# Kernel tuning notes

Measured on AMD Instinct MI355X. Metric: run time of the kernel, lower is better.

## Reference

```python
import jax, jax.numpy as jnp
import numpy as np

GAMMA = 1.0


def setup_inputs() -> dict:
    key = jax.random.key(0)
    k1, k2, k3 = jax.random.split(key, 3)
    n_query, n_train, d = 8192, 8192, 512
    X = jax.random.normal(k1, (n_query, d), dtype=jnp.float32)
    train_X = jax.random.normal(k2, (n_train, d), dtype=jnp.float32)
    dual_coef = jax.random.normal(k3, (n_train,), dtype=jnp.float32)
    return {"X": X, "train_X": train_X, "dual_coef": dual_coef}


def _rbf_kernel(x, y, gamma):
    x2 = jnp.sum(x * x, axis=-1, keepdims=True)          # (n_x, 1)
    y2 = jnp.sum(y * y, axis=-1)[None, :]                # (1, n_y)
    sq_dist = x2 + y2 - 2.0 * jnp.einsum('qd,td->qt', x, y)
    sq_dist = jnp.maximum(sq_dist, 0.0)                  # guard tiny negatives
    return jnp.exp(-gamma * sq_dist)                     # (n_x, n_y)


def reference(X, train_X, dual_coef):
    K_test = _rbf_kernel(X, train_X, GAMMA)              # (n_query, n_train)
    return K_test @ dual_coef                            # (n_query,)
```

## Files before the change

### kernel.cpp

```cpp
#include <hip/hip_runtime.h>
#include <hip/hip_bf16.h>
#include <stdint.h>

#define NQ 8192
#define NT 8192
#define DIM 512
#define BK 32
#define NKT (DIM / BK)
#define BM 256
#define BN 256
#define BUF_ELEMS ((BM + BN) * BK)

typedef __hip_bfloat16 bf16;
using bf16x8  = __attribute__((ext_vector_type(8))) short;
using f32x4   = __attribute__((ext_vector_type(4))) float;
using short8v = __attribute__((ext_vector_type(8))) short;

typedef __attribute__((address_space(1))) void* gas1_t;
typedef __attribute__((address_space(3))) void* las3_t;

__global__ void zero_out_k(float* __restrict__ out) {
    out[blockIdx.x * 256 + threadIdx.x] = 0.0f;
}

__global__ void prep_k(const float* __restrict__ X, const float* __restrict__ T,
                       bf16* __restrict__ Xb, bf16* __restrict__ Tb,
                       float* __restrict__ x2, float* __restrict__ y2) {
    const int w    = threadIdx.x >> 6;
    const int lane = threadIdx.x & 63;
    const int wid  = blockIdx.x * 4 + w;
#pragma unroll
    for (int rr = 0; rr < 2; ++rr) {
        const int row = wid * 2 + rr;
        const float* src; bf16* dst; float* nrm; int r;
        if (row < NQ) { r = row;      src = X + (size_t)r * DIM; dst = Xb + (size_t)r * DIM; nrm = x2; }
        else          { r = row - NQ; src = T + (size_t)r * DIM; dst = Tb + (size_t)r * DIM; nrm = y2; }
        const float4 v0 = reinterpret_cast<const float4*>(src)[lane * 2];
        const float4 v1 = reinterpret_cast<const float4*>(src)[lane * 2 + 1];
        float s = v0.x*v0.x + v0.y*v0.y + v0.z*v0.z + v0.w*v0.w
                + v1.x*v1.x + v1.y*v1.y + v1.z*v1.z + v1.w*v1.w;
        short8v pk;
        pk[0] = (short)__bfloat16_as_ushort(__float2bfloat16(v0.x));
        pk[1] = (short)__bfloat16_as_ushort(__float2bfloat16(v0.y));
        pk[2] = (short)__bfloat16_as_ushort(__float2bfloat16(v0.z));
        pk[3] = (short)__bfloat16_as_ushort(__float2bfloat16(v0.w));
        pk[4] = (short)__bfloat16_as_ushort(__float2bfloat16(v1.x));
        pk[5] = (short)__bfloat16_as_ushort(__float2bfloat16(v1.y));
        pk[6] = (short)__bfloat16_as_ushort(__float2bfloat16(v1.z));
        pk[7] = (short)__bfloat16_as_ushort(__float2bfloat16(v1.w));
        reinterpret_cast<short8v*>(dst)[lane] = pk;
#pragma unroll
        for (int off = 32; off; off >>= 1) s += __shfl_xor(s, off, 64);
        if (lane == 0) nrm[r] = s;
    }
}

__device__ __forceinline__ void stage_tile(
    const bf16* __restrict__ Tb, const bf16* __restrict__ Xb,
    int tBlk, int qBlk, int kt, bf16* sA, bf16* sB, int w, int lane) {
    const int k0 = kt * BK;
    const int rl = lane >> 2;
    const int sw = (rl >> 1) & 3;
    const int c  = (lane & 3) ^ sw;
#pragma unroll
    for (int j = 0; j < 2; ++j) {
        const int R0 = j * 128 + w * 16;
        const int R  = R0 + rl;
        const bf16* ga = Tb + (size_t)(tBlk + R) * DIM + k0 + c * 8;
        __builtin_amdgcn_global_load_lds((gas1_t)ga, (las3_t)(sA + R0 * BK), 16, 0, 0);
        const bf16* gb = Xb + (size_t)(qBlk + R) * DIM + k0 + c * 8;
        __builtin_amdgcn_global_load_lds((gas1_t)gb, (las3_t)(sB + R0 * BK), 16, 0, 0);
    }
}

__device__ __forceinline__ void compute_tile(
    const bf16* sA, const bf16* sB, int wm, int wn, int lane, f32x4 (&acc)[8][4]) {
    const int fr = lane & 15;
    const int fc = lane >> 4;
    const int swz = (fc ^ ((fr >> 1) & 3)) * 8;
    bf16x8 a[8], b[4];
#pragma unroll
    for (int m = 0; m < 8; ++m) {
        const int R = wm * 128 + m * 16 + fr;
        a[m] = *reinterpret_cast<const bf16x8*>(sA + R * BK + swz);
    }
#pragma unroll
    for (int n = 0; n < 4; ++n) {
        const int R = wn * 64 + n * 16 + fr;
        b[n] = *reinterpret_cast<const bf16x8*>(sB + R * BK + swz);
    }
    __builtin_amdgcn_s_setprio(1);
#pragma unroll
    for (int m = 0; m < 8; ++m)
#pragma unroll
        for (int n = 0; n < 4; ++n)
            acc[m][n] = __builtin_amdgcn_mfma_f32_16x16x32_bf16(a[m], b[n], acc[m][n], 0, 0, 0);
    __builtin_amdgcn_s_setprio(0);
}

#define WAIT_BAR(N)                                              \
    asm volatile("s_waitcnt vmcnt(" #N ")" ::: "memory");        \
    __builtin_amdgcn_s_barrier();                                \
    __builtin_amdgcn_sched_barrier(0);

__global__ __launch_bounds__(512, 2) void krr_mfma_k(
    const bf16* __restrict__ Tb, const bf16* __restrict__ Xb,
    const float* __restrict__ x2, const float* __restrict__ y2,
    const float* __restrict__ coef, float* __restrict__ out) {

    __shared__ bf16 lds[3 * BUF_ELEMS];

    const int tid  = threadIdx.x;
    const int w    = tid >> 6;
    const int lane = tid & 63;
    const int wm   = w >> 2;
    const int wn   = w & 3;

    const int qBlk = blockIdx.x * BN;
    const int tBlk = blockIdx.y * BM;

    f32x4 acc[8][4];
    const f32x4 z4 = {0.f, 0.f, 0.f, 0.f};
#pragma unroll
    for (int m = 0; m < 8; ++m)
#pragma unroll
        for (int n = 0; n < 4; ++n) acc[m][n] = z4;

    stage_tile(Tb, Xb, tBlk, qBlk, 0, lds,             lds + BM * BK,             w, lane);
    stage_tile(Tb, Xb, tBlk, qBlk, 1, lds + BUF_ELEMS, lds + BUF_ELEMS + BM * BK, w, lane);

    int bc = 0, bs = 2;
    for (int t = 0; t < NKT - 2; ++t) {
        WAIT_BAR(4)
        stage_tile(Tb, Xb, tBlk, qBlk, t + 2,
                   lds + bs * BUF_ELEMS, lds + bs * BUF_ELEMS + BM * BK, w, lane);
        compute_tile(lds + bc * BUF_ELEMS, lds + bc * BUF_ELEMS + BM * BK, wm, wn, lane, acc);
        bc = (bc == 2) ? 0 : bc + 1;
        bs = (bs == 2) ? 0 : bs + 1;
    }
    WAIT_BAR(4)
    compute_tile(lds + bc * BUF_ELEMS, lds + bc * BUF_ELEMS + BM * BK, wm, wn, lane, acc);
    bc = (bc == 2) ? 0 : bc + 1;
    WAIT_BAR(0)
    compute_tile(lds + bc * BUF_ELEMS, lds + bc * BUF_ELEMS + BM * BK, wm, wn, lane, acc);

    float s[4], x2q[4];
#pragma unroll
    for (int n = 0; n < 4; ++n) {
        s[n]   = 0.f;
        x2q[n] = x2[qBlk + wn * 64 + n * 16 + (lane & 15)];
    }
#pragma unroll
    for (int m = 0; m < 8; ++m) {
        const int tb = tBlk + wm * 128 + m * 16 + ((lane >> 4) << 2);
        float y2v[4], cfv[4];
#pragma unroll
        for (int r = 0; r < 4; ++r) { y2v[r] = y2[tb + r]; cfv[r] = coef[tb + r]; }
#pragma unroll
        for (int n = 0; n < 4; ++n)
#pragma unroll
            for (int r = 0; r < 4; ++r) {
                const float d  = acc[m][n][r];
                const float sq = fmaxf(x2q[n] + y2v[r] - 2.0f * d, 0.f);
                s[n] += __expf(-sq) * cfv[r];
            }
    }
#pragma unroll
    for (int n = 0; n < 4; ++n) {
        float v = s[n];
        v += __shfl_xor(v, 16, 64);
        v += __shfl_xor(v, 32, 64);
        if (lane < 16) atomicAdd(&out[qBlk + wn * 64 + n * 16 + lane], v);
    }
}

__global__ void krr_naive_k(const float* __restrict__ X, const float* __restrict__ T,
                            const float* __restrict__ coef, float* __restrict__ out) {
    __shared__ float xq[DIM];
    const int q = blockIdx.x;
    for (int i = threadIdx.x; i < DIM; i += 256) xq[i] = X[(size_t)q * DIM + i];
    __syncthreads();
    float s2 = 0.f;
    for (int i = 0; i < DIM; ++i) s2 += xq[i] * xq[i];
    float acc = 0.f;
    for (int t = threadIdx.x; t < NT; t += 256) {
        const float* ty = T + (size_t)t * DIM;
        float dot = 0.f, yy = 0.f;
        for (int i = 0; i < DIM; ++i) { float yv = ty[i]; dot += xq[i] * yv; yy += yv * yv; }
        float sq = fmaxf(s2 + yy - 2.0f * dot, 0.f);
        acc += __expf(-sq) * coef[t];
    }
#pragma unroll
    for (int off = 32; off > 0; off >>= 1) acc += __shfl_down(acc, off, 64);
    __shared__ float red[4];
    if ((threadIdx.x & 63) == 0) red[threadIdx.x >> 6] = acc;
    __syncthreads();
    if (threadIdx.x == 0) out[q] = red[0] + red[1] + red[2] + red[3];
}

extern "C" void kernel_launch(void* const* d_in, const int* in_sizes, int n_in,
                              void* d_out, int out_size, void* d_ws, size_t ws_size,
                              hipStream_t stream) {
    const float* X    = (const float*)d_in[0];
    const float* T    = (const float*)d_in[1];
    const float* coef = (const float*)d_in[2];
    float* out = (float*)d_out;

    zero_out_k<<<NQ / 256, 256, 0, stream>>>(out);

    const size_t need = (size_t)(NQ + NT) * DIM * sizeof(bf16) + (size_t)(NQ + NT) * sizeof(float);
    if (ws_size >= need) {
        bf16* Xb  = (bf16*)d_ws;
        bf16* Tb  = Xb + (size_t)NQ * DIM;
        float* x2 = (float*)(Tb + (size_t)NT * DIM);
        float* y2 = x2 + NQ;
        prep_k<<<2048, 256, 0, stream>>>(X, T, Xb, Tb, x2, y2);
        dim3 grid(NQ / BN, NT / BM);
        krr_mfma_k<<<grid, 512, 0, stream>>>(Tb, Xb, x2, y2, coef, out);
    } else {
        krr_naive_k<<<NQ, 256, 0, stream>>>(X, T, coef, out);
    }
}
```

Baseline: 149.9 us.

## Switch to 32x32 MFMA with BK=64 double buffer and quadrant-interleaved staging

```diff
diff --git a/kernel.cpp b/kernel.cpp
--- a/kernel.cpp
+++ b/kernel.cpp
@@ -5,15 +5,14 @@
 #define NQ 8192
 #define NT 8192
 #define DIM 512
-#define BK 32
+#define BK 64
 #define NKT (DIM / BK)
 #define BM 256
 #define BN 256
-#define BUF_ELEMS ((BM + BN) * BK)
 
 typedef __hip_bfloat16 bf16;
 using bf16x8  = __attribute__((ext_vector_type(8))) short;
-using f32x4   = __attribute__((ext_vector_type(4))) float;
+using f32x16  = __attribute__((ext_vector_type(16))) float;
 using short8v = __attribute__((ext_vector_type(8))) short;
 
 typedef __attribute__((address_space(1))) void* gas1_t;
@@ -55,60 +54,122 @@
     }
 }
 
-__device__ __forceinline__ void stage_tile(
+__device__ __forceinline__ void stage_half(
+    const bf16* __restrict__ src, int rowBase, int kt, bf16* dstHalf, int w, int lane) {
+    const int k0 = kt * BK;
+    const int rl = lane >> 3;
+    const int cl = (lane & 7) ^ rl;
+#pragma unroll
+    for (int j = 0; j < 2; ++j) {
+        const int R0 = w * 16 + j * 8;
+        const bf16* g = src + (size_t)(rowBase + R0 + rl) * DIM + k0 + cl * 8;
+        __builtin_amdgcn_global_load_lds((gas1_t)g, (las3_t)(dstHalf + R0 * BK), 16, 0, 0);
+    }
+}
+
+__device__ __forceinline__ bf16x8 lds_frag(const bf16* buf, int row, int ks, int kg) {
+    const int cl = ks * 2 + kg;
+    return *reinterpret_cast<const bf16x8*>(buf + row * BK + ((cl ^ (row & 7)) << 3));
+}
+
+#define MFMA32(A, B, C) __builtin_amdgcn_mfma_f32_32x32x16_bf16(A, B, C, 0, 0, 0)
+
+template<bool ST12, bool ST34, int VMC>
+__device__ __forceinline__ void segment(
     const bf16* __restrict__ Tb, const bf16* __restrict__ Xb,
-    int tBlk, int qBlk, int kt, bf16* sA, bf16* sB, int w, int lane) {
-    const int k0 = kt * BK;
-    const int rl = lane >> 2;
-    const int sw = (rl >> 1) & 3;
-    const int c  = (lane & 3) ^ sw;
-#pragma unroll
-    for (int j = 0; j < 2; ++j) {
-        const int R0 = j * 128 + w * 16;
-        const int R  = R0 + rl;
-        const bf16* ga = Tb + (size_t)(tBlk + R) * DIM + k0 + c * 8;
-        __builtin_amdgcn_global_load_lds((gas1_t)ga, (las3_t)(sA + R0 * BK), 16, 0, 0);
-        const bf16* gb = Xb + (size_t)(qBlk + R) * DIM + k0 + c * 8;
-        __builtin_amdgcn_global_load_lds((gas1_t)gb, (las3_t)(sB + R0 * BK), 16, 0, 0);
-    }
-}
-
-__device__ __forceinline__ void compute_tile(
-    const bf16* sA, const bf16* sB, int wm, int wn, int lane, f32x4 (&acc)[8][4]) {
-    const int fr = lane & 15;
-    const int fc = lane >> 4;
-    const int swz = (fc ^ ((fr >> 1) & 3)) * 8;
-    bf16x8 a[8], b[4];
-#pragma unroll
-    for (int m = 0; m < 8; ++m) {
-        const int R = wm * 128 + m * 16 + fr;
-        a[m] = *reinterpret_cast<const bf16x8*>(sA + R * BK + swz);
-    }
-#pragma unroll
-    for (int n = 0; n < 4; ++n) {
-        const int R = wn * 64 + n * 16 + fr;
-        b[n] = *reinterpret_cast<const bf16x8*>(sB + R * BK + swz);
-    }
-    __builtin_amdgcn_s_setprio(1);
-#pragma unroll
-    for (int m = 0; m < 8; ++m)
-#pragma unroll
-        for (int n = 0; n < 4; ++n)
-            acc[m][n] = __builtin_amdgcn_mfma_f32_16x16x32_bf16(a[m], b[n], acc[m][n], 0, 0, 0);
-    __builtin_amdgcn_s_setprio(0);
-}
-
-#define WAIT_BAR(N)                                              \
-    asm volatile("s_waitcnt vmcnt(" #N ")" ::: "memory");        \
-    __builtin_amdgcn_s_barrier();                                \
-    __builtin_amdgcn_sched_barrier(0);
+    int tBlk, int qBlk, bf16* bufC, bf16* bufN, int s,
+    int wm, int wn, int w, int lane, f32x16 (&acc)[4][2]) {
+
+    const bf16* cA = bufC;
+    const bf16* cB = bufC + 16384;
+    bf16* nA = bufN;
+    bf16* nB = bufN + 16384;
+    const int l31 = lane & 31;
+    const int kg  = lane >> 5;
+
+    bf16x8 aF[2][4], b0[4], b1[4];
+
+#pragma unroll
+    for (int mi = 0; mi < 2; ++mi) {
+        const int row = wm * 64 + mi * 32 + l31;
+#pragma unroll
+        for (int ks = 0; ks < 4; ++ks) aF[mi][ks] = lds_frag(cA, row, ks, kg);
+    }
+    {
+        const int row = wn * 32 + l31;
+#pragma unroll
+        for (int ks = 0; ks < 4; ++ks) b0[ks] = lds_frag(cB, row, ks, kg);
+    }
+    if (ST12) stage_half(Tb, tBlk + 128, s + 1, nA + 8192, w, lane);
+    __builtin_amdgcn_s_barrier();
+    asm volatile("s_waitcnt lgkmcnt(0)" ::: "memory");
+    __builtin_amdgcn_sched_barrier(0);
+    __builtin_amdgcn_s_setprio(1);
+#pragma unroll
+    for (int ks = 0; ks < 4; ++ks) {
+        acc[0][0] = MFMA32(aF[0][ks], b0[ks], acc[0][0]);
+        acc[1][0] = MFMA32(aF[1][ks], b0[ks], acc[1][0]);
+    }
+    __builtin_amdgcn_s_setprio(0);
+    __builtin_amdgcn_s_barrier();
+
+    {
+        const int row = 128 + wn * 32 + l31;
+#pragma unroll
+        for (int ks = 0; ks < 4; ++ks) b1[ks] = lds_frag(cB, row, ks, kg);
+    }
+    if (ST12) stage_half(Xb, qBlk + 0, s + 1, nB + 0, w, lane);
+    __builtin_amdgcn_s_barrier();
+    asm volatile("s_waitcnt lgkmcnt(0)" ::: "memory");
+    __builtin_amdgcn_sched_barrier(0);
+    __builtin_amdgcn_s_setprio(1);
+#pragma unroll
+    for (int ks = 0; ks < 4; ++ks) {
+        acc[0][1] = MFMA32(aF[0][ks], b1[ks], acc[0][1]);
+        acc[1][1] = MFMA32(aF[1][ks], b1[ks], acc[1][1]);
+    }
+    __builtin_amdgcn_s_setprio(0);
+    __builtin_amdgcn_s_barrier();
+
+#pragma unroll
+    for (int mi = 0; mi < 2; ++mi) {
+        const int row = 128 + wm * 64 + mi * 32 + l31;
+#pragma unroll
+        for (int ks = 0; ks < 4; ++ks) aF[mi][ks] = lds_frag(cA, row, ks, kg);
+    }
+    if (ST34) stage_half(Tb, tBlk + 0, s + 2, bufC + 0, w, lane);
+    __builtin_amdgcn_s_barrier();
+    asm volatile("s_waitcnt lgkmcnt(0)" ::: "memory");
+    __builtin_amdgcn_sched_barrier(0);
+    __builtin_amdgcn_s_setprio(1);
+#pragma unroll
+    for (int ks = 0; ks < 4; ++ks) {
+        acc[2][1] = MFMA32(aF[0][ks], b1[ks], acc[2][1]);
+        acc[3][1] = MFMA32(aF[1][ks], b1[ks], acc[3][1]);
+    }
+    __builtin_amdgcn_s_setprio(0);
+    __builtin_amdgcn_s_barrier();
+
+    if (ST34) stage_half(Xb, qBlk + 128, s + 2, bufC + 16384 + 8192, w, lane);
+    __builtin_amdgcn_s_setprio(1);
+#pragma unroll
+    for (int ks = 0; ks < 4; ++ks) {
+        acc[2][0] = MFMA32(aF[0][ks], b0[ks], acc[2][0]);
+        acc[3][0] = MFMA32(aF[1][ks], b0[ks], acc[3][0]);
+    }
+    __builtin_amdgcn_s_setprio(0);
+    if (VMC == 4)      asm volatile("s_waitcnt vmcnt(4)" ::: "memory");
+    else if (VMC == 0) asm volatile("s_waitcnt vmcnt(0)" ::: "memory");
+    __builtin_amdgcn_s_barrier();
+    __builtin_amdgcn_sched_barrier(0);
+}
 
 __global__ __launch_bounds__(512, 2) void krr_mfma_k(
     const bf16* __restrict__ Tb, const bf16* __restrict__ Xb,
     const float* __restrict__ x2, const float* __restrict__ y2,
     const float* __restrict__ coef, float* __restrict__ out) {
 
-    __shared__ bf16 lds[3 * BUF_ELEMS];
+    __shared__ bf16 lds[2 * 32768];
 
     const int tid  = threadIdx.x;
     const int w    = tid >> 6;
@@ -119,58 +180,62 @@
     const int qBlk = blockIdx.x * BN;
     const int tBlk = blockIdx.y * BM;
 
-    f32x4 acc[8][4];
-    const f32x4 z4 = {0.f, 0.f, 0.f, 0.f};
-#pragma unroll
-    for (int m = 0; m < 8; ++m)
-#pragma unroll
-        for (int n = 0; n < 4; ++n) acc[m][n] = z4;
-
-    stage_tile(Tb, Xb, tBlk, qBlk, 0, lds,             lds + BM * BK,             w, lane);
-    stage_tile(Tb, Xb, tBlk, qBlk, 1, lds + BUF_ELEMS, lds + BUF_ELEMS + BM * BK, w, lane);
-
-    int bc = 0, bs = 2;
-    for (int t = 0; t < NKT - 2; ++t) {
-        WAIT_BAR(4)
-        stage_tile(Tb, Xb, tBlk, qBlk, t + 2,
-                   lds + bs * BUF_ELEMS, lds + bs * BUF_ELEMS + BM * BK, w, lane);
-        compute_tile(lds + bc * BUF_ELEMS, lds + bc * BUF_ELEMS + BM * BK, wm, wn, lane, acc);
-        bc = (bc == 2) ? 0 : bc + 1;
-        bs = (bs == 2) ? 0 : bs + 1;
-    }
-    WAIT_BAR(4)
-    compute_tile(lds + bc * BUF_ELEMS, lds + bc * BUF_ELEMS + BM * BK, wm, wn, lane, acc);
-    bc = (bc == 2) ? 0 : bc + 1;
-    WAIT_BAR(0)
-    compute_tile(lds + bc * BUF_ELEMS, lds + bc * BUF_ELEMS + BM * BK, wm, wn, lane, acc);
-
-    float s[4], x2q[4];
-#pragma unroll
-    for (int n = 0; n < 4; ++n) {
-        s[n]   = 0.f;
-        x2q[n] = x2[qBlk + wn * 64 + n * 16 + (lane & 15)];
-    }
-#pragma unroll
-    for (int m = 0; m < 8; ++m) {
-        const int tb = tBlk + wm * 128 + m * 16 + ((lane >> 4) << 2);
-        float y2v[4], cfv[4];
-#pragma unroll
-        for (int r = 0; r < 4; ++r) { y2v[r] = y2[tb + r]; cfv[r] = coef[tb + r]; }
-#pragma unroll
-        for (int n = 0; n < 4; ++n)
-#pragma unroll
-            for (int r = 0; r < 4; ++r) {
-                const float d  = acc[m][n][r];
-                const float sq = fmaxf(x2q[n] + y2v[r] - 2.0f * d, 0.f);
-                s[n] += __expf(-sq) * cfv[r];
-            }
-    }
-#pragma unroll
-    for (int n = 0; n < 4; ++n) {
-        float v = s[n];
-        v += __shfl_xor(v, 16, 64);
-        v += __shfl_xor(v, 32, 64);
-        if (lane < 16) atomicAdd(&out[qBlk + wn * 64 + n * 16 + lane], v);
+    bf16* b0 = lds;
+    bf16* b1 = lds + 32768;
+
+    f32x16 acc[4][2];
+#pragma unroll
+    for (int mi = 0; mi < 4; ++mi)
+#pragma unroll
+        for (int ni = 0; ni < 2; ++ni)
+#pragma unroll
+            for (int r = 0; r < 16; ++r) acc[mi][ni][r] = 0.f;
+
+    stage_half(Tb, tBlk + 0,   0, b0 + 0,             w, lane);
+    stage_half(Xb, qBlk + 128, 0, b0 + 16384 + 8192,  w, lane);
+    stage_half(Tb, tBlk + 128, 0, b0 + 8192,          w, lane);
+    stage_half(Xb, qBlk + 0,   0, b0 + 16384,         w, lane);
+    stage_half(Tb, tBlk + 0,   1, b1 + 0,             w, lane);
+    stage_half(Xb, qBlk + 128, 1, b1 + 16384 + 8192,  w, lane);
+    asm volatile("s_waitcnt vmcnt(4)" ::: "memory");
+    __builtin_amdgcn_s_barrier();
+    __builtin_amdgcn_sched_barrier(0);
+
+#pragma unroll 1
+    for (int it = 0; it < 3; ++it) {
+        segment<true, true, 4>(Tb, Xb, tBlk, qBlk, b0, b1, 2 * it,     wm, wn, w, lane, acc);
+        segment<true, true, 4>(Tb, Xb, tBlk, qBlk, b1, b0, 2 * it + 1, wm, wn, w, lane, acc);
+    }
+    segment<true,  false, 0>(Tb, Xb, tBlk, qBlk, b0, b1, 6, wm, wn, w, lane, acc);
+    segment<false, false, -1>(Tb, Xb, tBlk, qBlk, b1, b0, 7, wm, wn, w, lane, acc);
+
+    const int l31 = lane & 31;
+    const int q0  = qBlk + wn * 32 + l31;
+    const int q1  = q0 + 128;
+    const float x2q0 = x2[q0];
+    const float x2q1 = x2[q1];
+    float s0 = 0.f, s1 = 0.f;
+#pragma unroll
+    for (int mi = 0; mi < 4; ++mi) {
+        const int tb = tBlk + (mi >> 1) * 128 + wm * 64 + (mi & 1) * 32 + 4 * (lane >> 5);
+        float y2v[16], cfv[16];
+#pragma unroll
+        for (int r = 0; r < 16; ++r) {
+            const int t = tb + (r & 3) + 8 * (r >> 2);
+            y2v[r] = y2[t];
+            cfv[r] = coef[t];
+        }
+#pragma unroll
+        for (int r = 0; r < 16; ++r) {
+            s0 += __expf(-fmaxf(x2q0 + y2v[r] - 2.0f * acc[mi][0][r], 0.f)) * cfv[r];
+            s1 += __expf(-fmaxf(x2q1 + y2v[r] - 2.0f * acc[mi][1][r], 0.f)) * cfv[r];
+        }
+    }
+    s0 += __shfl_xor(s0, 32, 64);
+    s1 += __shfl_xor(s1, 32, 64);
+    if (lane < 32) {
+        atomicAdd(&out[q0], s0);
+        atomicAdd(&out[q1], s1);
     }
 }
 
```

Result: slower. 165.0 us (+10.1%).

## Split each K-tile into two MFMA phases interleaving LDS reads and global staging

Applied to the files above, without the earlier changes.

```diff
diff --git a/kernel.cpp b/kernel.cpp
--- a/kernel.cpp
+++ b/kernel.cpp
@@ -9,6 +9,7 @@
 #define NKT (DIM / BK)
 #define BM 256
 #define BN 256
+#define AELEMS (BM * BK)
 #define BUF_ELEMS ((BM + BN) * BK)
 
 typedef __hip_bfloat16 bf16;
@@ -55,53 +56,74 @@
     }
 }
 
-__device__ __forceinline__ void stage_tile(
-    const bf16* __restrict__ Tb, const bf16* __restrict__ Xb,
-    int tBlk, int qBlk, int kt, bf16* sA, bf16* sB, int w, int lane) {
+__device__ __forceinline__ void stage_rows(
+    const bf16* __restrict__ src, int rowBase, int kt, bf16* dst, int w, int lane) {
     const int k0 = kt * BK;
     const int rl = lane >> 2;
-    const int sw = (rl >> 1) & 3;
-    const int c  = (lane & 3) ^ sw;
+    const int c  = (lane & 3) ^ ((rl >> 1) & 3);
 #pragma unroll
     for (int j = 0; j < 2; ++j) {
-        const int R0 = j * 128 + w * 16;
-        const int R  = R0 + rl;
-        const bf16* ga = Tb + (size_t)(tBlk + R) * DIM + k0 + c * 8;
-        __builtin_amdgcn_global_load_lds((gas1_t)ga, (las3_t)(sA + R0 * BK), 16, 0, 0);
-        const bf16* gb = Xb + (size_t)(qBlk + R) * DIM + k0 + c * 8;
-        __builtin_amdgcn_global_load_lds((gas1_t)gb, (las3_t)(sB + R0 * BK), 16, 0, 0);
-    }
-}
-
-__device__ __forceinline__ void compute_tile(
-    const bf16* sA, const bf16* sB, int wm, int wn, int lane, f32x4 (&acc)[8][4]) {
+        const int R0 = w * 32 + j * 16;
+        const bf16* g = src + (size_t)(rowBase + R0 + rl) * DIM + k0 + c * 8;
+        __builtin_amdgcn_global_load_lds((gas1_t)g, (las3_t)(dst + R0 * BK), 16, 0, 0);
+    }
+}
+
+__device__ __forceinline__ bf16x8 frag(const bf16* base, int row, int fc) {
+    return *reinterpret_cast<const bf16x8*>(
+        base + row * BK + ((fc ^ ((row >> 1) & 3)) << 3));
+}
+
+#define MFMA16(A, B, C) __builtin_amdgcn_mfma_f32_16x16x32_bf16(A, B, C, 0, 0, 0)
+
+template<bool ST, int VMC>
+__device__ __forceinline__ void ktile(
+    const bf16* __restrict__ Tb, const bf16* __restrict__ Xb,
+    int tBlk, int qBlk, int tS, const bf16* bufC, bf16* bufS,
+    int wm, int wn, int w, int lane, f32x4 (&acc)[8][4]) {
+
+    const bf16* cA = bufC;
+    const bf16* cB = bufC + AELEMS;
     const int fr = lane & 15;
     const int fc = lane >> 4;
-    const int swz = (fc ^ ((fr >> 1) & 3)) * 8;
-    bf16x8 a[8], b[4];
-#pragma unroll
-    for (int m = 0; m < 8; ++m) {
-        const int R = wm * 128 + m * 16 + fr;
-        a[m] = *reinterpret_cast<const bf16x8*>(sA + R * BK + swz);
-    }
-#pragma unroll
-    for (int n = 0; n < 4; ++n) {
-        const int R = wn * 64 + n * 16 + fr;
-        b[n] = *reinterpret_cast<const bf16x8*>(sB + R * BK + swz);
-    }
+
+    bf16x8 a[4], b[4];
+
+#pragma unroll
+    for (int m = 0; m < 4; ++m) a[m] = frag(cA, wm * 128 + m * 16 + fr, fc);
+#pragma unroll
+    for (int n = 0; n < 4; ++n) b[n] = frag(cB, wn * 64 + n * 16 + fr, fc);
+    if (ST) stage_rows(Tb, tBlk, tS, bufS, w, lane);
+    __builtin_amdgcn_s_barrier();
+    asm volatile("s_waitcnt lgkmcnt(0)" ::: "memory");
+    __builtin_amdgcn_sched_barrier(0);
     __builtin_amdgcn_s_setprio(1);
 #pragma unroll
-    for (int m = 0; m < 8; ++m)
+    for (int m = 0; m < 4; ++m)
 #pragma unroll
         for (int n = 0; n < 4; ++n)
-            acc[m][n] = __builtin_amdgcn_mfma_f32_16x16x32_bf16(a[m], b[n], acc[m][n], 0, 0, 0);
+            acc[m][n] = MFMA16(a[m], b[n], acc[m][n]);
     __builtin_amdgcn_s_setprio(0);
-}
-
-#define WAIT_BAR(N)                                              \
-    asm volatile("s_waitcnt vmcnt(" #N ")" ::: "memory");        \
-    __builtin_amdgcn_s_barrier();                                \
-    __builtin_amdgcn_sched_barrier(0);
+    __builtin_amdgcn_s_barrier();
+
+#pragma unroll
+    for (int m = 0; m < 4; ++m) a[m] = frag(cA, wm * 128 + (m + 4) * 16 + fr, fc);
+    if (ST) stage_rows(Xb, qBlk, tS, bufS + AELEMS, w, lane);
+    __builtin_amdgcn_s_barrier();
+    asm volatile("s_waitcnt lgkmcnt(0)" ::: "memory");
+    __builtin_amdgcn_sched_barrier(0);
+    __builtin_amdgcn_s_setprio(1);
+#pragma unroll
+    for (int m = 0; m < 4; ++m)
+#pragma unroll
+        for (int n = 0; n < 4; ++n)
+            acc[m + 4][n] = MFMA16(a[m], b[n], acc[m + 4][n]);
+    __builtin_amdgcn_s_setprio(0);
+    if (VMC == 4)      asm volatile("s_waitcnt vmcnt(4)" ::: "memory");
+    else if (VMC == 0) asm volatile("s_waitcnt vmcnt(0)" ::: "memory");
+    __builtin_amdgcn_s_barrier();
+    __builtin_amdgcn_sched_barrier(0);
+}
 
 __global__ __launch_bounds__(512, 2) void krr_mfma_k(
     const bf16* __restrict__ Tb, const bf16* __restrict__ Xb,
@@ -126,23 +148,27 @@
 #pragma unroll
         for (int n = 0; n < 4; ++n) acc[m][n] = z4;
 
-    stage_tile(Tb, Xb, tBlk, qBlk, 0, lds,             lds + BM * BK,             w, lane);
-    stage_tile(Tb, Xb, tBlk, qBlk, 1, lds + BUF_ELEMS, lds + BUF_ELEMS + BM * BK, w, lane);
-
-    int bc = 0, bs = 2;
+    stage_rows(Tb, tBlk, 0, lds, w, lane);
+    stage_rows(Xb, qBlk, 0, lds + AELEMS, w, lane);
+    stage_rows(Tb, tBlk, 1, lds + BUF_ELEMS, w, lane);
+    stage_rows(Xb, qBlk, 1, lds + BUF_ELEMS + AELEMS, w, lane);
+    asm volatile("s_waitcnt vmcnt(4)" ::: "memory");
+    __builtin_amdgcn_s_barrier();
+    __builtin_amdgcn_sched_barrier(0);
+
+    int bc = 0;
+#pragma unroll 1
     for (int t = 0; t < NKT - 2; ++t) {
-        WAIT_BAR(4)
-        stage_tile(Tb, Xb, tBlk, qBlk, t + 2,
-                   lds + bs * BUF_ELEMS, lds + bs * BUF_ELEMS + BM * BK, w, lane);
-        compute_tile(lds + bc * BUF_ELEMS, lds + bc * BUF_ELEMS + BM * BK, wm, wn, lane, acc);
+        const int bs = (bc == 0) ? 2 : bc - 1;
+        ktile<true, 4>(Tb, Xb, tBlk, qBlk, t + 2,
+                       lds + bc * BUF_ELEMS, lds + bs * BUF_ELEMS, wm, wn, w, lane, acc);
         bc = (bc == 2) ? 0 : bc + 1;
-        bs = (bs == 2) ? 0 : bs + 1;
-    }
-    WAIT_BAR(4)
-    compute_tile(lds + bc * BUF_ELEMS, lds + bc * BUF_ELEMS + BM * BK, wm, wn, lane, acc);
+    }
+    ktile<false, 0>(Tb, Xb, tBlk, qBlk, 0,
+                    lds + bc * BUF_ELEMS, lds, wm, wn, w, lane, acc);
     bc = (bc == 2) ? 0 : bc + 1;
-    WAIT_BAR(0)
-    compute_tile(lds + bc * BUF_ELEMS, lds + bc * BUF_ELEMS + BM * BK, wm, wn, lane, acc);
+    ktile<false, -1>(Tb, Xb, tBlk, qBlk, 0,
+                     lds + bc * BUF_ELEMS, lds, wm, wn, w, lane, acc);
 
     float s[4], x2q[4];
 #pragma unroll
```

Result: slower. 155.2 us (+3.6%).
